# Kernel tuning notes

Measured on AMD Instinct MI355X. Metric: run time of the kernel, lower is better.

Reference implementation:

```python
import jax, jax.numpy as jnp
import numpy as np

N, D, M, E, K = 16384, 512, 1024, 8, 2
LOSS_COEF = 0.01
EPS = 1e-10


def setup_inputs() -> dict:
    key = jax.random.key(0)
    ks = jax.random.split(key, 6)
    x = jax.random.normal(ks[0], (N, D), dtype=jnp.float32)
    # gate weight (torch init is zeros; use small random so routing is non-degenerate)
    w_gate = 0.02 * jax.random.normal(ks[1], (D, E), dtype=jnp.float32)
    # stacked expert FFN params: Linear(D->M), GELU, Linear(M->D)
    W1 = jax.random.normal(ks[2], (E, D, M), dtype=jnp.float32) / np.sqrt(D)
    b1 = jnp.zeros((E, M), dtype=jnp.float32)
    W2 = jax.random.normal(ks[3], (E, M, D), dtype=jnp.float32) / np.sqrt(M)
    b2 = jnp.zeros((E, D), dtype=jnp.float32)
    return {"x": x, "w_gate": w_gate, "W1": W1, "b1": b1, "W2": W2, "b2": b2}


def _cv_squared(v):
    # torch .var() is unbiased (ddof=1)
    v = v.astype(jnp.float32)
    return jnp.var(v, ddof=1) / (jnp.mean(v) ** 2 + EPS)


def reference(x, w_gate, W1, b1, W2, b2):
    n = x.shape[0]
    # --- noisy_top_k_gating (eval path: no noise) ---
    logits = x @ w_gate                                  # [N, E]
    top_logits, top_idx = jax.lax.top_k(logits, min(K + 1, E))
    topk_logits = top_logits[:, :K]                      # [N, K]
    topk_idx = top_idx[:, :K]                            # [N, K]
    topk_gates = jax.nn.softmax(topk_logits, axis=-1)    # [N, K]
    gates = jnp.zeros_like(logits).at[jnp.arange(n)[:, None], topk_idx].set(topk_gates)
    importance = gates.sum(axis=0)                       # [E]
    load = (gates > 0).sum(axis=0).astype(jnp.float32)   # [E]
    loss = LOSS_COEF * (_cv_squared(importance) + _cv_squared(load))
    # --- experts (dense equivalent of sparse dispatch/combine: gate==0 rows contribute 0) ---
    h = jnp.einsum('nd,edm->enm', x, W1) + b1[:, None, :]     # [E, N, M]
    h = jax.nn.gelu(h, approximate=False)
    out = jnp.einsum('enm,emd->end', h, W2) + b2[:, None, :]  # [E, N, D]
    y = jnp.einsum('ne,end->nd', gates, out)                  # [N, D]
    return (y, loss)
```

## Files before the change

kernel.cpp:

```cpp
#include <hip/hip_runtime.h>
#include <math.h>

#define NTOK 16384
#define DDIM 512
#define MDIM 1024
#define NEXP 8
#define BKW 32
#define TMAX 264

typedef __attribute__((ext_vector_type(8))) short short8;
typedef __attribute__((ext_vector_type(4))) float floatx4;

__device__ inline unsigned short f2bf(float f){
  union { float f; unsigned int u; } v; v.f = f;
  unsigned int u = v.u;
  u += ((u >> 16) & 1u) + 0x7fffu;
  return (unsigned short)(u >> 16);
}

__device__ inline float bf2f(unsigned short s){
  union { unsigned int u; float f; } v;
  v.u = ((unsigned int)s) << 16;
  return v.f;
}

__device__ inline float gelu_fast(float x){
  float u = x * 0.70710678118654752f;
  float a = fabsf(u);
  float t = __builtin_amdgcn_rcpf(fmaf(0.3275911f, a, 1.0f));
  float p = fmaf(1.061405429f, t, -1.453152027f);
  p = fmaf(p, t, 1.421413741f);
  p = fmaf(p, t, -0.284496736f);
  p = fmaf(p, t, 0.254829592f);
  p = p * t;
  float e = __expf(-u * u);
  float erfa = fmaf(-p, e, 1.0f);
  float erfu = copysignf(erfa, u);
  return 0.5f * x * (1.0f + erfu);
}

__device__ __forceinline__ void gload16(const unsigned short* g, unsigned short* l){
  __builtin_amdgcn_global_load_lds(
      (const __attribute__((address_space(1))) void*)g,
      (__attribute__((address_space(3))) void*)l,
      16, 0, 0);
}


__global__ void init_small_kernel(int* counts, float* imp){
  int t = threadIdx.x;
  if (t < NEXP){ counts[t] = 0; imp[t] = 0.0f; }
}

__global__ void transpose_conv_kernel(const float* __restrict__ in,
                                      unsigned short* __restrict__ out,
                                      int R, int C){
  __shared__ float tile[32][33];
  int e  = blockIdx.z;
  int c0 = blockIdx.x << 5;
  int r0 = blockIdx.y << 5;
  const float* src = in + (size_t)e * R * C;
  unsigned short* dst = out + (size_t)e * R * C;
  int tc = threadIdx.x;
  int tr = threadIdx.y;
  #pragma unroll
  for (int i = 0; i < 32; i += 8)
    tile[tr + i][tc] = src[(size_t)(r0 + tr + i) * C + c0 + tc];
  __syncthreads();
  #pragma unroll
  for (int i = 0; i < 32; i += 8)
    dst[(size_t)(c0 + tr + i) * R + r0 + tc] = f2bf(tile[tc][tr + i]);
}


__global__ __launch_bounds__(256)
void gating_kernel(const float* __restrict__ x,
                   const float* __restrict__ wg,
                   unsigned short* __restrict__ xb,
                   int* __restrict__ tok_e, float* __restrict__ tok_g,
                   int* __restrict__ counts, float* __restrict__ imp){
  __shared__ int   lcnt[NEXP];
  __shared__ float limp[NEXP];
  int t = threadIdx.x;
  if (t < NEXP){ lcnt[t] = 0; limp[t] = 0.0f; }
  __syncthreads();

  int wave = t >> 6;
  int lane = t & 63;

  for (int it = 0; it < 4; it++){
    int n = blockIdx.x * 16 + it * 4 + wave;

    const float4* xp = (const float4*)(x + (size_t)n * DDIM + lane * 8);
    float4 a = xp[0], b = xp[1];
    float xv[8] = {a.x, a.y, a.z, a.w, b.x, b.y, b.z, b.w};

    short8 xo;
    #pragma unroll
    for (int j = 0; j < 8; j++) xo[j] = (short)f2bf(xv[j]);
    *(short8*)(xb + (size_t)n * DDIM + lane * 8) = xo;

    double acc[NEXP];
    #pragma unroll
    for (int e = 0; e < NEXP; e++) acc[e] = 0.0;
    #pragma unroll
    for (int j = 0; j < 8; j++){
      const float* wr = wg + (size_t)(lane * 8 + j) * NEXP;
      #pragma unroll
      for (int e = 0; e < NEXP; e++) acc[e] += (double)xv[j] * (double)wr[e];
    }
    #pragma unroll
    for (int off = 32; off >= 1; off >>= 1){
      #pragma unroll
      for (int e = 0; e < NEXP; e++) acc[e] += __shfl_xor(acc[e], off);
    }
    if (lane == 0){
      int i0 = -1, i1 = -1;
      double l0 = -1e300, l1 = -1e300;
      #pragma unroll
      for (int e = 0; e < NEXP; e++){
        double v = acc[e];
        if (v > l0){ l1 = l0; i1 = i0; l0 = v; i0 = e; }
        else if (v > l1){ l1 = v; i1 = e; }
      }
      float ex = expf((float)(l1 - l0));
      float g0 = 1.0f / (1.0f + ex);
      float g1 = ex / (1.0f + ex);
      tok_e[n * 2]     = i0; tok_e[n * 2 + 1] = i1;
      tok_g[n * 2]     = g0; tok_g[n * 2 + 1] = g1;
      atomicAdd(&lcnt[i0], 1); atomicAdd(&lcnt[i1], 1);
      atomicAdd(&limp[i0], g0); atomicAdd(&limp[i1], g1);
    }
  }
  __syncthreads();
  if (t < NEXP){
    atomicAdd(&counts[t], lcnt[t]);
    atomicAdd(&imp[t], limp[t]);
  }
}

__global__ void loss_scan_kernel(const int* __restrict__ counts,
                                 const float* __restrict__ imp,
                                 int* __restrict__ offsets, int* __restrict__ cursor,
                                 int* __restrict__ tile_pre,
                                 float* __restrict__ out_loss){
  int l = threadIdx.x;
  int   c  = (l < NEXP) ? counts[l] : 0;
  float im = (l < NEXP) ? imp[l]    : 0.0f;
  int   tl = (c + 127) >> 7;

  int poff = 0, ptl = 0;
  int tot = 0, tott = 0;
  double si = 0, si2 = 0, sl = 0, sl2 = 0;
  #pragma unroll
  for (int e = 0; e < NEXP; e++){
    int   ce = __shfl(c, e);
    int   te = __shfl(tl, e);
    float ie = __shfl(im, e);
    if (e < l){ poff += ce; ptl += te; }
    tot += ce; tott += te;
    si += (double)ie; si2 += (double)ie * ie;
    sl += (double)ce; sl2 += (double)ce * ce;
  }
  if (l < NEXP){ offsets[l] = poff; cursor[l] = poff; tile_pre[l] = ptl; }
  if (l == 0){
    offsets[NEXP] = tot; tile_pre[NEXP] = tott;
    double mi = si / 8.0, ml = sl / 8.0;
    double vi = (si2 - 8.0 * mi * mi) / 7.0;
    double vl = (sl2 - 8.0 * ml * ml) / 7.0;
    *out_loss = (float)(0.01 * (vi / (mi * mi + 1e-10) + vl / (ml * ml + 1e-10)));
  }
}

__global__ __launch_bounds__(256)
void scatter_kernel(const int* __restrict__ tok_e,
                    int* __restrict__ cursor,
                    int* __restrict__ btok, int* __restrict__ slot_of){
  __shared__ int lcnt[NEXP];
  __shared__ int lbase[NEXP];
  int t = threadIdx.x;
  if (t < NEXP) lcnt[t] = 0;
  __syncthreads();

  int n = blockIdx.x * 256 + t;
  int e0 = tok_e[n * 2], e1 = tok_e[n * 2 + 1];
  int r0 = atomicAdd(&lcnt[e0], 1);
  int r1 = atomicAdd(&lcnt[e1], 1);
  __syncthreads();
  if (t < NEXP) lbase[t] = atomicAdd(&cursor[t], lcnt[t]);
  __syncthreads();
  int s0 = lbase[e0] + r0;
  int s1 = lbase[e1] + r1;
  btok[s0] = n;
  btok[s1] = n;
  slot_of[n * 2]     = s0;
  slot_of[n * 2 + 1] = s1;
}


__global__ __launch_bounds__(512, 6)
void gemm1_kernel(const unsigned short* __restrict__ xb,
                  const unsigned short* __restrict__ w1t,
                  const float* __restrict__ b1,
                  const int* __restrict__ offsets,
                  const int* __restrict__ tile_pre,
                  const int* __restrict__ btok,
                  unsigned short* __restrict__ H){
  int b = blockIdx.x;
  int L = (b & 7) * TMAX + (b >> 3);
  int ct = L & 7;
  int tt = L >> 3;
  if (tt >= tile_pre[NEXP]) return;
  int e = 0;
  while (tt >= tile_pre[e + 1]) e++;
  int rt = tt - tile_pre[e];
  int off = offsets[e];
  int cnt = offsets[e + 1] - off;
  int r0 = rt << 7;

  __shared__ unsigned short As[3 * 128 * BKW];
  __shared__ unsigned short Bs[3 * 128 * BKW];

  int t = threadIdx.x;
  int w = t >> 6;
  int l = t & 63;
  int g = (l & 3) ^ ((l >> 3) & 3);

  const unsigned short* apt;
  {
    int ra = r0 + w * 16 + (l >> 2);  if (ra >= cnt) ra = cnt - 1;
    apt = xb + (size_t)btok[off + ra] * DDIM + g * 8;
  }
  const unsigned short* bpt = w1t + ((size_t)e * MDIM + (ct << 7) + w * 16 + (l >> 2)) * DDIM + g * 8;

  int wr = (w >> 1) << 5;
  int wc = (w & 1) << 6;
  int lm = l & 15;
  int lq = l >> 4;
  int swz = (lm >> 1) & 3;

  int aoff[2], boff[4];
  #pragma unroll
  for (int i = 0; i < 2; i++) aoff[i] = (wr + i * 16 + lm) * BKW + ((lq ^ swz) << 3);
  #pragma unroll
  for (int j = 0; j < 4; j++) boff[j] = (wc + j * 16 + lm) * BKW + ((lq ^ swz) << 3);

  floatx4 acc[2][4] = {};

  #define STAGE1(K0, CB) {                                   \
    gload16(apt + (K0), As + (CB) * 4096 + w * 512);         \
    gload16(bpt + (K0), Bs + (CB) * 4096 + w * 512);         \
  }
  #define READ1(CB) {                                        \
    const unsigned short* Ac = As + (CB) * 4096;             \
    const unsigned short* Bc = Bs + (CB) * 4096;             \
    _Pragma("unroll")                                        \
    for (int i = 0; i < 2; i++) af[i]  = *(const short8*)(Ac + aoff[i]); \
    _Pragma("unroll")                                        \
    for (int j = 0; j < 4; j++) bfr[j] = *(const short8*)(Bc + boff[j]); \
  }
  #define MFMA1 {                                            \
    _Pragma("unroll")                                        \
    for (int i = 0; i < 2; i++)                              \
      _Pragma("unroll")                                      \
      for (int j = 0; j < 4; j++)                            \
        acc[i][j] = __builtin_amdgcn_mfma_f32_16x16x32_bf16(af[i], bfr[j], acc[i][j], 0, 0, 0); \
  }
  #define WAITBAR(N) {                                       \
    asm volatile("s_waitcnt vmcnt(" #N ")" ::: "memory");    \
    __builtin_amdgcn_sched_barrier(0);                       \
    __builtin_amdgcn_s_barrier();                            \
    __builtin_amdgcn_sched_barrier(0);                       \
  }

  const int NK = DDIM / BKW;
  STAGE1(0, 0);
  STAGE1(BKW, 1);
  WAITBAR(2);
  #pragma unroll
  for (int k = 0; k < NK; k++){
    const int cur = k % 3;
    short8 af[2], bfr[4];
    READ1(cur);
    if (k < NK - 2) STAGE1((k + 2) * BKW, (k + 2) % 3);
    __builtin_amdgcn_s_setprio(1);
    MFMA1;
    __builtin_amdgcn_s_setprio(0);
    if (k < NK - 2){ WAITBAR(2); }
    else if (k == NK - 2){ WAITBAR(0); }
  }
  #undef STAGE1
  #undef READ1
  #undef MFMA1
  #undef WAITBAR

  const float* bias = b1 + e * MDIM + (ct << 7);
  #pragma unroll
  for (int i = 0; i < 2; i++){
    int rbase = wr + i * 16 + lq * 4;
    #pragma unroll
    for (int j = 0; j < 4; j++){
      int cc = wc + j * 16 + lm;
      float bv = bias[cc];
      #pragma unroll
      for (int r = 0; r < 4; r++){
        int row = r0 + rbase + r;
        if (row < cnt){
          float v = acc[i][j][r] + bv;
          H[(size_t)(off + row) * MDIM + (ct << 7) + cc] = f2bf(gelu_fast(v));
        }
      }
    }
  }
}

__global__ __launch_bounds__(512, 6)
void gemm2_kernel(const unsigned short* __restrict__ H,
                  const unsigned short* __restrict__ w2t,
                  const float* __restrict__ b2,
                  const int* __restrict__ offsets,
                  const int* __restrict__ tile_pre,
                  unsigned short* __restrict__ O){
  int b = blockIdx.x;
  int L = (b & 7) * (TMAX / 2) + (b >> 3);
  int ct = L & 3;
  int tt = L >> 2;
  if (tt >= tile_pre[NEXP]) return;
  int e = 0;
  while (tt >= tile_pre[e + 1]) e++;
  int rt = tt - tile_pre[e];
  int off = offsets[e];
  int cnt = offsets[e + 1] - off;
  int r0 = rt << 7;

  __shared__ unsigned short As[3 * 128 * BKW];
  __shared__ unsigned short Bs[3 * 128 * BKW];

  int t = threadIdx.x;
  int w = t >> 6;
  int l = t & 63;
  int g = (l & 3) ^ ((l >> 3) & 3);

  const unsigned short* apt;
  {
    int ra = r0 + w * 16 + (l >> 2);  if (ra >= cnt) ra = cnt - 1;
    apt = H + (size_t)(off + ra) * MDIM + g * 8;
  }
  const unsigned short* bpt = w2t + ((size_t)e * DDIM + (ct << 7) + w * 16 + (l >> 2)) * MDIM + g * 8;

  int wr = (w >> 1) << 5;
  int wc = (w & 1) << 6;
  int lm = l & 15;
  int lq = l >> 4;
  int swz = (lm >> 1) & 3;

  int aoff[2], boff[4];
  #pragma unroll
  for (int i = 0; i < 2; i++) aoff[i] = (wr + i * 16 + lm) * BKW + ((lq ^ swz) << 3);
  #pragma unroll
  for (int j = 0; j < 4; j++) boff[j] = (wc + j * 16 + lm) * BKW + ((lq ^ swz) << 3);

  floatx4 acc[2][4] = {};

  #define STAGE2(K0, CB) {                                   \
    gload16(apt + (K0), As + (CB) * 4096 + w * 512);         \
    gload16(bpt + (K0), Bs + (CB) * 4096 + w * 512);         \
  }
  #define READ2(CB) {                                        \
    const unsigned short* Ac = As + (CB) * 4096;             \
    const unsigned short* Bc = Bs + (CB) * 4096;             \
    _Pragma("unroll")                                        \
    for (int i = 0; i < 2; i++) af[i]  = *(const short8*)(Ac + aoff[i]); \
    _Pragma("unroll")                                        \
    for (int j = 0; j < 4; j++) bfr[j] = *(const short8*)(Bc + boff[j]); \
  }
  #define MFMA2 {                                            \
    _Pragma("unroll")                                        \
    for (int i = 0; i < 2; i++)                              \
      _Pragma("unroll")                                      \
      for (int j = 0; j < 4; j++)                            \
        acc[i][j] = __builtin_amdgcn_mfma_f32_16x16x32_bf16(af[i], bfr[j], acc[i][j], 0, 0, 0); \
  }
  #define WAITBAR2(N) {                                      \
    asm volatile("s_waitcnt vmcnt(" #N ")" ::: "memory");    \
    __builtin_amdgcn_sched_barrier(0);                       \
    __builtin_amdgcn_s_barrier();                            \
    __builtin_amdgcn_sched_barrier(0);                       \
  }

  const int NK = MDIM / BKW;
  STAGE2(0, 0);
  STAGE2(BKW, 1);
  WAITBAR2(2);
  #pragma unroll
  for (int k = 0; k < NK; k++){
    const int cur = k % 3;
    short8 af[2], bfr[4];
    READ2(cur);
    if (k < NK - 2) STAGE2((k + 2) * BKW, (k + 2) % 3);
    __builtin_amdgcn_s_setprio(1);
    MFMA2;
    __builtin_amdgcn_s_setprio(0);
    if (k < NK - 2){ WAITBAR2(2); }
    else if (k == NK - 2){ WAITBAR2(0); }
  }
  #undef STAGE2
  #undef READ2
  #undef MFMA2
  #undef WAITBAR2

  const float* bias = b2 + e * DDIM + (ct << 7);
  #pragma unroll
  for (int i = 0; i < 2; i++){
    int rbase = wr + i * 16 + lq * 4;
    #pragma unroll
    for (int j = 0; j < 4; j++){
      int cc = wc + j * 16 + lm;
      float bv = bias[cc];
      #pragma unroll
      for (int r = 0; r < 4; r++){
        int row = r0 + rbase + r;
        if (row < cnt)
          O[(size_t)(off + row) * DDIM + (ct << 7) + cc] = f2bf(acc[i][j][r] + bv);
      }
    }
  }
}


__global__ __launch_bounds__(256)
void combine_kernel(const unsigned short* __restrict__ O,
                    const float* __restrict__ tok_g,
                    const int* __restrict__ slot_of,
                    float* __restrict__ y){
  int wave = threadIdx.x >> 6;
  int lane = threadIdx.x & 63;
  int n = blockIdx.x * 4 + wave;
  int s0 = slot_of[n * 2], s1 = slot_of[n * 2 + 1];
  float g0 = tok_g[n * 2], g1 = tok_g[n * 2 + 1];
  short8 a = *(const short8*)(O + (size_t)s0 * DDIM + lane * 8);
  short8 b = *(const short8*)(O + (size_t)s1 * DDIM + lane * 8);
  float4 o0, o1;
  float* po0 = (float*)&o0;
  float* po1 = (float*)&o1;
  #pragma unroll
  for (int j = 0; j < 4; j++){
    po0[j] = g0 * bf2f((unsigned short)a[j]) + g1 * bf2f((unsigned short)b[j]);
    po1[j] = g0 * bf2f((unsigned short)a[j + 4]) + g1 * bf2f((unsigned short)b[j + 4]);
  }
  float4* yp = (float4*)(y + (size_t)n * DDIM + lane * 8);
  yp[0] = o0;
  yp[1] = o1;
}


extern "C" void kernel_launch(void* const* d_in, const int* in_sizes, int n_in,
                              void* d_out, int out_size, void* d_ws, size_t ws_size,
                              hipStream_t stream){
  const float* x  = (const float*)d_in[0];
  const float* wg = (const float*)d_in[1];
  const float* W1 = (const float*)d_in[2];
  const float* b1 = (const float*)d_in[3];
  const float* W2 = (const float*)d_in[4];
  const float* b2 = (const float*)d_in[5];
  float* y = (float*)d_out;

  char* ws = (char*)d_ws;
  size_t o = 0;
  auto alloc = [&](size_t bytes)->char*{
    char* p = ws + o;
    o += (bytes + 255) & ~(size_t)255;
    return p;
  };
  unsigned short* xb   = (unsigned short*)alloc((size_t)NTOK * DDIM * 2);
  unsigned short* w1t  = (unsigned short*)alloc((size_t)NEXP * MDIM * DDIM * 2);
  unsigned short* w2t  = (unsigned short*)alloc((size_t)NEXP * DDIM * MDIM * 2);
  unsigned short* H    = (unsigned short*)alloc((size_t)NTOK * 2 * MDIM * 2);
  unsigned short* O    = (unsigned short*)alloc((size_t)NTOK * 2 * DDIM * 2);
  int*   btok    = (int*)  alloc((size_t)NTOK * 2 * 4);
  int*   slot_of = (int*)  alloc((size_t)NTOK * 2 * 4);
  int*   tok_e   = (int*)  alloc((size_t)NTOK * 2 * 4);
  float* tok_g   = (float*)alloc((size_t)NTOK * 2 * 4);
  int*   counts  = (int*)  alloc(64);
  float* imp     = (float*)alloc(64);
  int*   offsets = (int*)  alloc(64);
  int*   cursor  = (int*)  alloc(64);
  int*   tile_pre= (int*)  alloc(64);

  hipLaunchKernelGGL(init_small_kernel, dim3(1), dim3(64), 0, stream, counts, imp);
  hipLaunchKernelGGL(transpose_conv_kernel, dim3(MDIM / 32, DDIM / 32, NEXP), dim3(32, 8), 0, stream,
                     W1, w1t, DDIM, MDIM);
  hipLaunchKernelGGL(transpose_conv_kernel, dim3(DDIM / 32, MDIM / 32, NEXP), dim3(32, 8), 0, stream,
                     W2, w2t, MDIM, DDIM);
  hipLaunchKernelGGL(gating_kernel, dim3(NTOK / 16), dim3(256), 0, stream,
                     x, wg, xb, tok_e, tok_g, counts, imp);
  hipLaunchKernelGGL(loss_scan_kernel, dim3(1), dim3(64), 0, stream,
                     counts, imp, offsets, cursor, tile_pre, y + (size_t)NTOK * DDIM);
  hipLaunchKernelGGL(scatter_kernel, dim3(NTOK / 256), dim3(256), 0, stream,
                     tok_e, cursor, btok, slot_of);
  hipLaunchKernelGGL(gemm1_kernel, dim3(TMAX * 8), dim3(512), 0, stream,
                     xb, w1t, b1, offsets, tile_pre, btok, H);
  hipLaunchKernelGGL(gemm2_kernel, dim3(TMAX * 4), dim3(512), 0, stream,
                     H, w2t, b2, offsets, tile_pre, O);
  hipLaunchKernelGGL(combine_kernel, dim3(NTOK / 4), dim3(256), 0, stream,
                     O, tok_g, slot_of, y);
}
```

Before: 275.7 us.

## Widen expert GEMM tiles to 128x256 with 4x4 MFMA fragments per wave

Both expert GEMMs now compute 128x256 output tiles instead of 128x128. Each of the 8 waves owns a 64x64 sub-tile with 16 accumulators, and the B tile is staged as two 128-row halves. This halves the grid and raises arithmetic intensity per LDS byte and per A-tile load, cutting redundant gathers of token rows. In exchange it uses more registers and LDS, so occupancy drops to 4 blocks, and there are fewer blocks to balance across CUs.

Result: slower. 288.9 us (+4.8%).

```diff
diff --git a/kernel.cpp b/kernel.cpp
--- a/kernel.cpp
+++ b/kernel.cpp
@@ -198,7 +198,7 @@
 }
 
 
-__global__ __launch_bounds__(512, 6)
+__global__ __launch_bounds__(512, 4)
 void gemm1_kernel(const unsigned short* __restrict__ xb,
                   const unsigned short* __restrict__ w1t,
                   const float* __restrict__ b1,
@@ -207,9 +207,9 @@
                   const int* __restrict__ btok,
                   unsigned short* __restrict__ H){
   int b = blockIdx.x;
-  int L = (b & 7) * TMAX + (b >> 3);
-  int ct = L & 7;
-  int tt = L >> 3;
+  int L = (b & 7) * 132 + (b >> 3);
+  int ct = L & 3;
+  int tt = L >> 2;
   if (tt >= tile_pre[NEXP]) return;
   int e = 0;
   while (tt >= tile_pre[e + 1]) e++;
@@ -219,49 +219,51 @@
   int r0 = rt << 7;
 
   __shared__ unsigned short As[3 * 128 * BKW];
-  __shared__ unsigned short Bs[3 * 128 * BKW];
+  __shared__ unsigned short Bs[3 * 256 * BKW];
 
   int t = threadIdx.x;
   int w = t >> 6;
   int l = t & 63;
-  int g = (l & 3) ^ ((l >> 3) & 3);
+  int g = (t & 3) ^ ((t >> 3) & 3);
 
   const unsigned short* apt;
   {
-    int ra = r0 + w * 16 + (l >> 2);  if (ra >= cnt) ra = cnt - 1;
+    int ra = r0 + (t >> 2);  if (ra >= cnt) ra = cnt - 1;
     apt = xb + (size_t)btok[off + ra] * DDIM + g * 8;
   }
-  const unsigned short* bpt = w1t + ((size_t)e * MDIM + (ct << 7) + w * 16 + (l >> 2)) * DDIM + g * 8;
-
-  int wr = (w >> 1) << 5;
-  int wc = (w & 1) << 6;
+  const unsigned short* bpt0 = w1t + ((size_t)e * MDIM + (ct << 8) + (t >> 2)) * DDIM + g * 8;
+  const unsigned short* bpt1 = bpt0 + (size_t)128 * DDIM;
+
+  int wr = (w >> 2) << 6;
+  int wc = (w & 3) << 6;
   int lm = l & 15;
   int lq = l >> 4;
-  int swz = (lm >> 1) & 3;
-
-  int aoff[2], boff[4];
-  #pragma unroll
-  for (int i = 0; i < 2; i++) aoff[i] = (wr + i * 16 + lm) * BKW + ((lq ^ swz) << 3);
-  #pragma unroll
-  for (int j = 0; j < 4; j++) boff[j] = (wc + j * 16 + lm) * BKW + ((lq ^ swz) << 3);
-
-  floatx4 acc[2][4] = {};
+  int koff = ((lq ^ ((lm >> 1) & 3)) << 3);
+
+  int aoff[4], boff[4];
+  #pragma unroll
+  for (int i = 0; i < 4; i++) aoff[i] = (wr + i * 16 + lm) * BKW + koff;
+  #pragma unroll
+  for (int j = 0; j < 4; j++) boff[j] = (wc + j * 16 + lm) * BKW + koff;
+
+  floatx4 acc[4][4] = {};
 
   #define STAGE1(K0, CB) {                                   \
-    gload16(apt + (K0), As + (CB) * 4096 + w * 512);         \
-    gload16(bpt + (K0), Bs + (CB) * 4096 + w * 512);         \
+    gload16(apt  + (K0), As + (CB) * 4096 + w * 512);        \
+    gload16(bpt0 + (K0), Bs + (CB) * 8192 + w * 512);        \
+    gload16(bpt1 + (K0), Bs + (CB) * 8192 + 4096 + w * 512); \
   }
   #define READ1(CB) {                                        \
     const unsigned short* Ac = As + (CB) * 4096;             \
-    const unsigned short* Bc = Bs + (CB) * 4096;             \
+    const unsigned short* Bc = Bs + (CB) * 8192;             \
     _Pragma("unroll")                                        \
-    for (int i = 0; i < 2; i++) af[i]  = *(const short8*)(Ac + aoff[i]); \
+    for (int i = 0; i < 4; i++) af[i]  = *(const short8*)(Ac + aoff[i]); \
     _Pragma("unroll")                                        \
     for (int j = 0; j < 4; j++) bfr[j] = *(const short8*)(Bc + boff[j]); \
   }
   #define MFMA1 {                                            \
     _Pragma("unroll")                                        \
-    for (int i = 0; i < 2; i++)                              \
+    for (int i = 0; i < 4; i++)                              \
       _Pragma("unroll")                                      \
       for (int j = 0; j < 4; j++)                            \
         acc[i][j] = __builtin_amdgcn_mfma_f32_16x16x32_bf16(af[i], bfr[j], acc[i][j], 0, 0, 0); \
@@ -276,17 +278,17 @@
   const int NK = DDIM / BKW;
   STAGE1(0, 0);
   STAGE1(BKW, 1);
-  WAITBAR(2);
+  WAITBAR(3);
   #pragma unroll
   for (int k = 0; k < NK; k++){
     const int cur = k % 3;
-    short8 af[2], bfr[4];
+    short8 af[4], bfr[4];
     READ1(cur);
     if (k < NK - 2) STAGE1((k + 2) * BKW, (k + 2) % 3);
     __builtin_amdgcn_s_setprio(1);
     MFMA1;
     __builtin_amdgcn_s_setprio(0);
-    if (k < NK - 2){ WAITBAR(2); }
+    if (k < NK - 2){ WAITBAR(3); }
     else if (k == NK - 2){ WAITBAR(0); }
   }
   #undef STAGE1
@@ -294,9 +296,9 @@
   #undef MFMA1
   #undef WAITBAR
 
-  const float* bias = b1 + e * MDIM + (ct << 7);
-  #pragma unroll
-  for (int i = 0; i < 2; i++){
+  const float* bias = b1 + e * MDIM + (ct << 8);
+  #pragma unroll
+  for (int i = 0; i < 4; i++){
     int rbase = wr + i * 16 + lq * 4;
     #pragma unroll
     for (int j = 0; j < 4; j++){
@@ -307,14 +309,14 @@
         int row = r0 + rbase + r;
         if (row < cnt){
           float v = acc[i][j][r] + bv;
-          H[(size_t)(off + row) * MDIM + (ct << 7) + cc] = f2bf(gelu_fast(v));
+          H[(size_t)(off + row) * MDIM + (ct << 8) + cc] = f2bf(gelu_fast(v));
         }
       }
     }
   }
 }
 
-__global__ __launch_bounds__(512, 6)
+__global__ __launch_bounds__(512, 4)
 void gemm2_kernel(const unsigned short* __restrict__ H,
                   const unsigned short* __restrict__ w2t,
                   const float* __restrict__ b2,
@@ -322,9 +324,9 @@
                   const int* __restrict__ tile_pre,
                   unsigned short* __restrict__ O){
   int b = blockIdx.x;
-  int L = (b & 7) * (TMAX / 2) + (b >> 3);
-  int ct = L & 3;
-  int tt = L >> 2;
+  int L = (b & 7) * 66 + (b >> 3);
+  int ct = L & 1;
+  int tt = L >> 1;
   if (tt >= tile_pre[NEXP]) return;
   int e = 0;
   while (tt >= tile_pre[e + 1]) e++;
@@ -334,49 +336,51 @@
   int r0 = rt << 7;
 
   __shared__ unsigned short As[3 * 128 * BKW];
-  __shared__ unsigned short Bs[3 * 128 * BKW];
+  __shared__ unsigned short Bs[3 * 256 * BKW];
 
   int t = threadIdx.x;
   int w = t >> 6;
   int l = t & 63;
-  int g = (l & 3) ^ ((l >> 3) & 3);
+  int g = (t & 3) ^ ((t >> 3) & 3);
 
   const unsigned short* apt;
   {
-    int ra = r0 + w * 16 + (l >> 2);  if (ra >= cnt) ra = cnt - 1;
+    int ra = r0 + (t >> 2);  if (ra >= cnt) ra = cnt - 1;
     apt = H + (size_t)(off + ra) * MDIM + g * 8;
   }
-  const unsigned short* bpt = w2t + ((size_t)e * DDIM + (ct << 7) + w * 16 + (l >> 2)) * MDIM + g * 8;
-
-  int wr = (w >> 1) << 5;
-  int wc = (w & 1) << 6;
+  const unsigned short* bpt0 = w2t + ((size_t)e * DDIM + (ct << 8) + (t >> 2)) * MDIM + g * 8;
+  const unsigned short* bpt1 = bpt0 + (size_t)128 * MDIM;
+
+  int wr = (w >> 2) << 6;
+  int wc = (w & 3) << 6;
   int lm = l & 15;
   int lq = l >> 4;
-  int swz = (lm >> 1) & 3;
-
-  int aoff[2], boff[4];
-  #pragma unroll
-  for (int i = 0; i < 2; i++) aoff[i] = (wr + i * 16 + lm) * BKW + ((lq ^ swz) << 3);
-  #pragma unroll
-  for (int j = 0; j < 4; j++) boff[j] = (wc + j * 16 + lm) * BKW + ((lq ^ swz) << 3);
-
-  floatx4 acc[2][4] = {};
+  int koff = ((lq ^ ((lm >> 1) & 3)) << 3);
+
+  int aoff[4], boff[4];
+  #pragma unroll
+  for (int i = 0; i < 4; i++) aoff[i] = (wr + i * 16 + lm) * BKW + koff;
+  #pragma unroll
+  for (int j = 0; j < 4; j++) boff[j] = (wc + j * 16 + lm) * BKW + koff;
+
+  floatx4 acc[4][4] = {};
 
   #define STAGE2(K0, CB) {                                   \
-    gload16(apt + (K0), As + (CB) * 4096 + w * 512);         \
-    gload16(bpt + (K0), Bs + (CB) * 4096 + w * 512);         \
+    gload16(apt  + (K0), As + (CB) * 4096 + w * 512);        \
+    gload16(bpt0 + (K0), Bs + (CB) * 8192 + w * 512);        \
+    gload16(bpt1 + (K0), Bs + (CB) * 8192 + 4096 + w * 512); \
   }
   #define READ2(CB) {                                        \
     const unsigned short* Ac = As + (CB) * 4096;             \
-    const unsigned short* Bc = Bs + (CB) * 4096;             \
+    const unsigned short* Bc = Bs + (CB) * 8192;             \
     _Pragma("unroll")                                        \
-    for (int i = 0; i < 2; i++) af[i]  = *(const short8*)(Ac + aoff[i]); \
+    for (int i = 0; i < 4; i++) af[i]  = *(const short8*)(Ac + aoff[i]); \
     _Pragma("unroll")                                        \
     for (int j = 0; j < 4; j++) bfr[j] = *(const short8*)(Bc + boff[j]); \
   }
   #define MFMA2 {                                            \
     _Pragma("unroll")                                        \
-    for (int i = 0; i < 2; i++)                              \
+    for (int i = 0; i < 4; i++)                              \
       _Pragma("unroll")                                      \
       for (int j = 0; j < 4; j++)                            \
         acc[i][j] = __builtin_amdgcn_mfma_f32_16x16x32_bf16(af[i], bfr[j], acc[i][j], 0, 0, 0); \
@@ -391,17 +395,17 @@
   const int NK = MDIM / BKW;
   STAGE2(0, 0);
   STAGE2(BKW, 1);
-  WAITBAR2(2);
+  WAITBAR2(3);
   #pragma unroll
   for (int k = 0; k < NK; k++){
     const int cur = k % 3;
-    short8 af[2], bfr[4];
+    short8 af[4], bfr[4];
     READ2(cur);
     if (k < NK - 2) STAGE2((k + 2) * BKW, (k + 2) % 3);
     __builtin_amdgcn_s_setprio(1);
     MFMA2;
     __builtin_amdgcn_s_setprio(0);
-    if (k < NK - 2){ WAITBAR2(2); }
+    if (k < NK - 2){ WAITBAR2(3); }
     else if (k == NK - 2){ WAITBAR2(0); }
   }
   #undef STAGE2
@@ -409,9 +413,9 @@
   #undef MFMA2
   #undef WAITBAR2
 
-  const float* bias = b2 + e * DDIM + (ct << 7);
-  #pragma unroll
-  for (int i = 0; i < 2; i++){
+  const float* bias = b2 + e * DDIM + (ct << 8);
+  #pragma unroll
+  for (int i = 0; i < 4; i++){
     int rbase = wr + i * 16 + lq * 4;
     #pragma unroll
     for (int j = 0; j < 4; j++){
@@ -421,7 +425,7 @@
       for (int r = 0; r < 4; r++){
         int row = r0 + rbase + r;
         if (row < cnt)
-          O[(size_t)(off + row) * DDIM + (ct << 7) + cc] = f2bf(acc[i][j][r] + bv);
+          O[(size_t)(off + row) * DDIM + (ct << 8) + cc] = f2bf(acc[i][j][r] + bv);
       }
     }
   }
@@ -498,9 +502,9 @@
                      counts, imp, offsets, cursor, tile_pre, y + (size_t)NTOK * DDIM);
   hipLaunchKernelGGL(scatter_kernel, dim3(NTOK / 256), dim3(256), 0, stream,
                      tok_e, cursor, btok, slot_of);
-  hipLaunchKernelGGL(gemm1_kernel, dim3(TMAX * 8), dim3(512), 0, stream,
+  hipLaunchKernelGGL(gemm1_kernel, dim3(TMAX * 4), dim3(512), 0, stream,
                      xb, w1t, b1, offsets, tile_pre, btok, H);
-  hipLaunchKernelGGL(gemm2_kernel, dim3(TMAX * 4), dim3(512), 0, stream,
+  hipLaunchKernelGGL(gemm2_kernel, dim3(TMAX * 2), dim3(512), 0, stream,
                      H, w2t, b2, offsets, tile_pre, O);
   hipLaunchKernelGGL(combine_kernel, dim3(NTOK / 4), dim3(256), 0, stream,
                      O, tok_g, slot_of, y);
```

## Fuse combine into gemm2 via atomic scatter-add and merge prep kernels

Applied to the files above, without the earlier changes.

Removes the combine kernel and the bf16 O buffer. gemm2 now scales each output row by its gate and atomically adds it into y, which gating_kernel zeroes first. The weight transposes and counter init are merged into a single prep kernel, cutting launches. The cost is two fp32 atomics per output element with scattered row addresses, and the summation order of the two expert contributions is no longer fixed.

Measured after the change: 280.5 us. Within noise of the previous version (+1.7%).

```diff
diff --git a/kernel.cpp b/kernel.cpp
--- a/kernel.cpp
+++ b/kernel.cpp
@@ -47,18 +47,18 @@
 }
 
 
-__global__ void init_small_kernel(int* counts, float* imp){
-  int t = threadIdx.x;
-  if (t < NEXP){ counts[t] = 0; imp[t] = 0.0f; }
-}
-
-__global__ void transpose_conv_kernel(const float* __restrict__ in,
-                                      unsigned short* __restrict__ out,
-                                      int R, int C){
+__global__ void prep_kernel(const float* __restrict__ W1, const float* __restrict__ W2,
+                            unsigned short* __restrict__ w1t, unsigned short* __restrict__ w2t,
+                            int* __restrict__ counts, float* __restrict__ imp){
   __shared__ float tile[32][33];
-  int e  = blockIdx.z;
-  int c0 = blockIdx.x << 5;
-  int r0 = blockIdx.y << 5;
+  int z = blockIdx.z;
+  if (z == 0 && blockIdx.x == 0 && blockIdx.y == 0){
+    int flat = threadIdx.y * 32 + threadIdx.x;
+    if (flat < NEXP){ counts[flat] = 0; imp[flat] = 0.0f; }
+  }
+  const float* in; unsigned short* out; int R, C, c0, r0, e;
+  if (z < 8){ e = z;     in = W1; out = w1t; R = DDIM; C = MDIM; c0 = blockIdx.x << 5; r0 = blockIdx.y << 5; }
+  else      { e = z - 8; in = W2; out = w2t; R = MDIM; C = DDIM; c0 = blockIdx.y << 5; r0 = blockIdx.x << 5; }
   const float* src = in + (size_t)e * R * C;
   unsigned short* dst = out + (size_t)e * R * C;
   int tc = threadIdx.x;
@@ -78,11 +78,19 @@
                    const float* __restrict__ wg,
                    unsigned short* __restrict__ xb,
                    int* __restrict__ tok_e, float* __restrict__ tok_g,
-                   int* __restrict__ counts, float* __restrict__ imp){
+                   int* __restrict__ counts, float* __restrict__ imp,
+                   float* __restrict__ y){
   __shared__ int   lcnt[NEXP];
   __shared__ float limp[NEXP];
   int t = threadIdx.x;
   if (t < NEXP){ lcnt[t] = 0; limp[t] = 0.0f; }
+
+  {
+    float4 z4 = {0.f, 0.f, 0.f, 0.f};
+    float4* yz = (float4*)(y + (size_t)blockIdx.x * 8192);
+    #pragma unroll
+    for (int i = 0; i < 8; i++) yz[t + i * 256] = z4;
+  }
   __syncthreads();
 
   int wave = t >> 6;
@@ -174,8 +182,9 @@
 
 __global__ __launch_bounds__(256)
 void scatter_kernel(const int* __restrict__ tok_e,
+                    const float* __restrict__ tok_g,
                     int* __restrict__ cursor,
-                    int* __restrict__ btok, int* __restrict__ slot_of){
+                    int* __restrict__ btok, float* __restrict__ slot_g){
   __shared__ int lcnt[NEXP];
   __shared__ int lbase[NEXP];
   int t = threadIdx.x;
@@ -193,8 +202,8 @@
   int s1 = lbase[e1] + r1;
   btok[s0] = n;
   btok[s1] = n;
-  slot_of[n * 2]     = s0;
-  slot_of[n * 2 + 1] = s1;
+  slot_g[s0] = tok_g[n * 2];
+  slot_g[s1] = tok_g[n * 2 + 1];
 }
 
 
@@ -320,7 +329,9 @@
                   const float* __restrict__ b2,
                   const int* __restrict__ offsets,
                   const int* __restrict__ tile_pre,
-                  unsigned short* __restrict__ O){
+                  const int* __restrict__ btok,
+                  const float* __restrict__ slot_g,
+                  float* __restrict__ y){
   int b = blockIdx.x;
   int L = (b & 7) * (TMAX / 2) + (b >> 3);
   int ct = L & 3;
@@ -410,47 +421,26 @@
   #undef WAITBAR2
 
   const float* bias = b2 + e * DDIM + (ct << 7);
+  float bv[4];
+  #pragma unroll
+  for (int j = 0; j < 4; j++) bv[j] = bias[wc + j * 16 + lm];
+
   #pragma unroll
   for (int i = 0; i < 2; i++){
     int rbase = wr + i * 16 + lq * 4;
     #pragma unroll
-    for (int j = 0; j < 4; j++){
-      int cc = wc + j * 16 + lm;
-      float bv = bias[cc];
-      #pragma unroll
-      for (int r = 0; r < 4; r++){
-        int row = r0 + rbase + r;
-        if (row < cnt)
-          O[(size_t)(off + row) * DDIM + (ct << 7) + cc] = f2bf(acc[i][j][r] + bv);
+    for (int r = 0; r < 4; r++){
+      int row = r0 + rbase + r;
+      if (row < cnt){
+        int tok   = btok[off + row];
+        float gg  = slot_g[off + row];
+        float* yr = y + (size_t)tok * DDIM + (ct << 7);
+        #pragma unroll
+        for (int j = 0; j < 4; j++)
+          atomicAdd(&yr[wc + j * 16 + lm], gg * (acc[i][j][r] + bv[j]));
       }
     }
   }
-}
-
-
-__global__ __launch_bounds__(256)
-void combine_kernel(const unsigned short* __restrict__ O,
-                    const float* __restrict__ tok_g,
-                    const int* __restrict__ slot_of,
-                    float* __restrict__ y){
-  int wave = threadIdx.x >> 6;
-  int lane = threadIdx.x & 63;
-  int n = blockIdx.x * 4 + wave;
-  int s0 = slot_of[n * 2], s1 = slot_of[n * 2 + 1];
-  float g0 = tok_g[n * 2], g1 = tok_g[n * 2 + 1];
-  short8 a = *(const short8*)(O + (size_t)s0 * DDIM + lane * 8);
-  short8 b = *(const short8*)(O + (size_t)s1 * DDIM + lane * 8);
-  float4 o0, o1;
-  float* po0 = (float*)&o0;
-  float* po1 = (float*)&o1;
-  #pragma unroll
-  for (int j = 0; j < 4; j++){
-    po0[j] = g0 * bf2f((unsigned short)a[j]) + g1 * bf2f((unsigned short)b[j]);
-    po1[j] = g0 * bf2f((unsigned short)a[j + 4]) + g1 * bf2f((unsigned short)b[j + 4]);
-  }
-  float4* yp = (float4*)(y + (size_t)n * DDIM + lane * 8);
-  yp[0] = o0;
-  yp[1] = o1;
 }
 
 
@@ -476,9 +466,8 @@
   unsigned short* w1t  = (unsigned short*)alloc((size_t)NEXP * MDIM * DDIM * 2);
   unsigned short* w2t  = (unsigned short*)alloc((size_t)NEXP * DDIM * MDIM * 2);
   unsigned short* H    = (unsigned short*)alloc((size_t)NTOK * 2 * MDIM * 2);
-  unsigned short* O    = (unsigned short*)alloc((size_t)NTOK * 2 * DDIM * 2);
   int*   btok    = (int*)  alloc((size_t)NTOK * 2 * 4);
-  int*   slot_of = (int*)  alloc((size_t)NTOK * 2 * 4);
+  float* slot_g  = (float*)alloc((size_t)NTOK * 2 * 4);
   int*   tok_e   = (int*)  alloc((size_t)NTOK * 2 * 4);
   float* tok_g   = (float*)alloc((size_t)NTOK * 2 * 4);
   int*   counts  = (int*)  alloc(64);
@@ -487,21 +476,16 @@
   int*   cursor  = (int*)  alloc(64);
   int*   tile_pre= (int*)  alloc(64);
 
-  hipLaunchKernelGGL(init_small_kernel, dim3(1), dim3(64), 0, stream, counts, imp);
-  hipLaunchKernelGGL(transpose_conv_kernel, dim3(MDIM / 32, DDIM / 32, NEXP), dim3(32, 8), 0, stream,
-                     W1, w1t, DDIM, MDIM);
-  hipLaunchKernelGGL(transpose_conv_kernel, dim3(DDIM / 32, MDIM / 32, NEXP), dim3(32, 8), 0, stream,
-                     W2, w2t, MDIM, DDIM);
+  hipLaunchKernelGGL(prep_kernel, dim3(32, 16, 16), dim3(32, 8), 0, stream,
+                     W1, W2, w1t, w2t, counts, imp);
   hipLaunchKernelGGL(gating_kernel, dim3(NTOK / 16), dim3(256), 0, stream,
-                     x, wg, xb, tok_e, tok_g, counts, imp);
+                     x, wg, xb, tok_e, tok_g, counts, imp, y);
   hipLaunchKernelGGL(loss_scan_kernel, dim3(1), dim3(64), 0, stream,
                      counts, imp, offsets, cursor, tile_pre, y + (size_t)NTOK * DDIM);
   hipLaunchKernelGGL(scatter_kernel, dim3(NTOK / 256), dim3(256), 0, stream,
-                     tok_e, cursor, btok, slot_of);
+                     tok_e, tok_g, cursor, btok, slot_g);
   hipLaunchKernelGGL(gemm1_kernel, dim3(TMAX * 8), dim3(512), 0, stream,
                      xb, w1t, b1, offsets, tile_pre, btok, H);
   hipLaunchKernelGGL(gemm2_kernel, dim3(TMAX * 4), dim3(512), 0, stream,
-                     H, w2t, b2, offsets, tile_pre, O);
-  hipLaunchKernelGGL(combine_kernel, dim3(NTOK / 4), dim3(256), 0, stream,
-                     O, tok_g, slot_of, y);
-}
+                     H, w2t, b2, offsets, tile_pre, btok, slot_g, y);
+}
```
